# Performance work log

Measured on AMD Instinct MI355X. Metric: run time of the kernel, lower is better.

## Reference

```python
import jax, jax.numpy as jnp
import numpy as np

B, S, D, H, DH = 2, 2048, 1024, 16, 64
EPS = 1e-6


def setup_inputs() -> dict:
    key = jax.random.key(0)
    k0, k1, k2 = jax.random.split(key, 3)
    x = jax.random.normal(k0, (B, S, D), dtype=jnp.float32)
    mask = jnp.ones((B, S), dtype=bool)
    # NeoX-style rotary angles: half-dim inverse freqs, duplicated to rot_dim=DH
    inv_freq = 1.0 / (10000.0 ** (jnp.arange(0, DH, 2, dtype=jnp.float32) / DH))  # [DH/2]
    ang = jnp.arange(S, dtype=jnp.float32)[:, None] * inv_freq[None, :]            # [S, DH/2]
    freqs = jnp.concatenate([ang, ang], axis=-1)                                    # [S, DH]
    W_qkv = jax.random.normal(k1, (3 * D, D), dtype=jnp.float32) * (D ** -0.5)
    W_out = jax.random.normal(k2, (D, D), dtype=jnp.float32) * (D ** -0.5)
    q_gamma = jnp.ones((DH,), jnp.float32)
    q_beta = jnp.zeros((DH,), jnp.float32)
    k_gamma = jnp.ones((DH,), jnp.float32)
    k_beta = jnp.zeros((DH,), jnp.float32)
    return {"x": x, "mask": mask, "freqs": freqs, "W_qkv": W_qkv, "W_out": W_out,
            "q_gamma": q_gamma, "q_beta": q_beta, "k_gamma": k_gamma, "k_beta": k_beta}


def _layernorm(t, g, b):
    mu = t.mean(-1, keepdims=True)
    var = t.var(-1, keepdims=True)
    return (t - mu) * jax.lax.rsqrt(var + EPS) * g + b


def _rotate_half(t):
    t1, t2 = jnp.split(t, 2, axis=-1)
    return jnp.concatenate([-t2, t1], axis=-1)


def reference(x, mask, freqs, W_qkv, W_out, q_gamma, q_beta, k_gamma, k_beta):
    b, s, d = x.shape
    # fused QKV projection + split into heads: b n (h d) -> b h n d
    qkv = x @ W_qkv.T                                   # [b, s, 3d]
    q, k, v = jnp.split(qkv, 3, axis=-1)
    to_heads = lambda t: t.reshape(b, s, H, DH).transpose(0, 2, 1, 3)
    q, k, v = to_heads(q), to_heads(k), to_heads(v)      # [b, h, s, dh]
    # qk layernorm
    q = _layernorm(q, q_gamma, q_beta)
    k = _layernorm(k, k_gamma, k_beta)
    # rotary embedding (fp32 path in the original; inputs already fp32)
    cos = jnp.cos(freqs)[None, None]                      # [1, 1, s, dh]
    sin = jnp.sin(freqs)[None, None]
    q = q * cos + _rotate_half(q) * sin
    k = k * cos + _rotate_half(k) * sin
    # mask construction: key padding mask 'b j -> b 1 1 j' combined with causal
    key_mask = mask[:, None, None, :]                     # [b, 1, 1, s]
    causal = jnp.tril(jnp.ones((s, s), dtype=bool))       # [s, s]
    comb = key_mask & causal[None, None]                  # [b, 1, s, s]
    row_masked = ~comb.any(axis=-1)                       # [b, 1, s]
    comb = comb.at[..., 0].set(comb[..., 0] | row_masked)
    # SDPA
    scale = DH ** -0.5
    scores = jnp.einsum('bhid,bhjd->bhij', q, k) * scale  # [b, h, s, s]
    scores = jnp.where(comb, scores, jnp.finfo(scores.dtype).min)
    attn = jax.nn.softmax(scores, axis=-1)
    out = jnp.einsum('bhij,bhjd->bhid', attn, v)          # [b, h, s, dh]
    out = jnp.where(row_masked[..., None], 0.0, out)
    # merge heads + output projection
    out = out.transpose(0, 2, 1, 3).reshape(b, s, d)
    return out @ W_out.T
```

## Files before the change

### kernel.cpp

```cpp
#include <hip/hip_runtime.h>
#include <hip/hip_bf16.h>
#include <cstdint>

typedef unsigned short u16;
typedef __attribute__((ext_vector_type(8))) short s16x8;
typedef __attribute__((ext_vector_type(4))) float f32x4;
typedef __attribute__((ext_vector_type(16))) float f32x16;
typedef __attribute__((ext_vector_type(4))) unsigned int u32x4;
typedef __attribute__((ext_vector_type(2))) unsigned int u32x2;
typedef __attribute__((ext_vector_type(4))) u16 u16x4;

#define LOG2E 1.44269504088896340736f

__device__ __forceinline__ u16 f2b(float f) {
  union { float f; unsigned u; } v; v.f = f;
  unsigned r = v.u + 0x7FFF + ((v.u >> 16) & 1);
  return (u16)(r >> 16);
}

__device__ __forceinline__ float b2f(u16 u) {
  union { unsigned u; float f; } v; v.u = ((unsigned)u) << 16;
  return v.f;
}

__device__ __forceinline__ void gload_lds16(const u16* g, u16* l) {
  __builtin_amdgcn_global_load_lds((const __attribute__((address_space(1))) void*)g,
                                   (__attribute__((address_space(3))) void*)l, 16, 0, 0);
}

__global__ void cvt_bf16(const float* __restrict__ in, u16* __restrict__ out, int n) {
  int i = blockIdx.x * blockDim.x + threadIdx.x;
  if (i < n) out[i] = f2b(in[i]);
}

__global__ void trig_tab(const float* __restrict__ f, float* __restrict__ c,
                         float* __restrict__ s, int n) {
  int i = blockIdx.x * blockDim.x + threadIdx.x;
  if (i < n) { c[i] = cosf(f[i]); s[i] = sinf(f[i]); }
}

__global__ __launch_bounds__(256) void gemm_bt(const u16* __restrict__ A, const u16* __restrict__ B,
                                               float* __restrict__ C, int M, int N, int K) {
  __shared__ u16 sA[128 * 64];
  __shared__ u16 sB[128 * 64];
  const int nbn = N >> 7;
  int bx = blockIdx.x % nbn, by = blockIdx.x / nbn;
  int tid = threadIdx.x, w = tid >> 6, lane = tid & 63;
  int wr = (w >> 1) * 64, wc = (w & 1) * 64;
  int lr = lane >> 3, lc = lane & 7;
  f32x4 acc[4][4] = {};
  size_t arow = (size_t)(by * 128) * K;
  size_t brow = (size_t)(bx * 128) * K;
  for (int k0 = 0; k0 < K; k0 += 64) {
    __syncthreads();
    for (int c = 0; c < 4; ++c) {
      int r = w * 32 + c * 8;
      gload_lds16(A + arow + (size_t)(r + lr) * K + k0 + lc * 8, &sA[r * 64]);
      gload_lds16(B + brow + (size_t)(r + lr) * K + k0 + lc * 8, &sB[r * 64]);
    }
    __syncthreads();
    for (int kk = 0; kk < 64; kk += 32) {
      s16x8 af[4], bf[4];
      int ro = lane & 15, ko = kk + (lane >> 4) * 8;
      for (int m = 0; m < 4; ++m) af[m] = *(const s16x8*)&sA[(wr + m * 16 + ro) * 64 + ko];
      for (int n = 0; n < 4; ++n) bf[n] = *(const s16x8*)&sB[(wc + n * 16 + ro) * 64 + ko];
      for (int m = 0; m < 4; ++m)
        for (int n = 0; n < 4; ++n)
          acc[m][n] = __builtin_amdgcn_mfma_f32_16x16x32_bf16(af[m], bf[n], acc[m][n], 0, 0, 0);
    }
  }
  int ro = lane & 15, rg = lane >> 4;
  for (int m = 0; m < 4; ++m)
    for (int n = 0; n < 4; ++n) {
      int row = by * 128 + wr + m * 16 + rg * 4;
      int col = bx * 128 + wc + n * 16 + ro;
      float* cp = C + (size_t)row * N + col;
      for (int r = 0; r < 4; ++r) cp[(size_t)r * N] = acc[m][n][r];
    }
}

__global__ __launch_bounds__(256) void ln_rope(const float* __restrict__ qkv,
    const float* __restrict__ cosT, const float* __restrict__ sinT,
    const float* __restrict__ qg, const float* __restrict__ qb,
    const float* __restrict__ kg, const float* __restrict__ kb,
    u16* __restrict__ qo, u16* __restrict__ ko, u16* __restrict__ vo) {
  int gw = (blockIdx.x * 256 + threadIdx.x) >> 6;
  int lane = threadIdx.x & 63;
  int h = gw & 15, bs = gw >> 4;
  int s = bs & 2047, b = bs >> 11;
  const float* row = qkv + (size_t)bs * 3072;
  float qv = row[h * 64 + lane];
  float kv = row[1024 + h * 64 + lane];
  float vv = row[2048 + h * 64 + lane];

  float s1q = qv, s2q = qv * qv, s1k = kv, s2k = kv * kv;
  for (int off = 1; off < 64; off <<= 1) {
    s1q += __shfl_xor(s1q, off, 64); s2q += __shfl_xor(s2q, off, 64);
    s1k += __shfl_xor(s1k, off, 64); s2k += __shfl_xor(s2k, off, 64);
  }
  float muq = s1q * (1.f / 64.f), varq = s2q * (1.f / 64.f) - muq * muq;
  float muk = s1k * (1.f / 64.f), vark = s2k * (1.f / 64.f) - muk * muk;
  float qn = (qv - muq) * rsqrtf(varq + 1e-6f) * qg[lane] + qb[lane];
  float kn = (kv - muk) * rsqrtf(vark + 1e-6f) * kg[lane] + kb[lane];

  float cs = cosT[s * 64 + lane], sn = sinT[s * 64 + lane];
  float qh = __shfl_xor(qn, 32, 64); qh = (lane < 32) ? -qh : qh;
  float kh = __shfl_xor(kn, 32, 64); kh = (lane < 32) ? -kh : kh;
  float qr = (qn * cs + qh * sn) * 0.125f;
  float kr = kn * cs + kh * sn;

  size_t oidx = ((size_t)((b * 16 + h) * 2048 + s)) * 64 + lane;
  qo[oidx] = f2b(qr); ko[oidx] = f2b(kr); vo[oidx] = f2b(vv);
}

__global__ __launch_bounds__(256) void transpose_v(const u16* __restrict__ vi, u16* __restrict__ vt) {
  __shared__ __align__(16) u16 tile[64][72];
  int bh = blockIdx.x >> 5, st = blockIdx.x & 31;
  int t = threadIdx.x;
  const u16* src = vi + ((size_t)bh * 2048 + st * 64) * 64;
  int r = t & 63, c = (t >> 6) * 16;
  *(s16x8*)&tile[r][c]     = *(const s16x8*)(src + r * 64 + c);
  *(s16x8*)&tile[r][c + 8] = *(const s16x8*)(src + r * 64 + c + 8);
  __syncthreads();
  int dh = t & 63, so = (t >> 6) * 16;
  alignas(16) u16 buf[16];
  #pragma unroll
  for (int j = 0; j < 16; ++j) buf[j] = tile[so + j][dh];
  u16* dst = vt + ((size_t)bh * 64 + dh) * 2048 + st * 64 + so;
  *(s16x8*)dst       = *(const s16x8*)&buf[0];
  *(s16x8*)(dst + 8) = *(const s16x8*)&buf[8];
}

__global__ __launch_bounds__(256) void attn_fwd6(const u16* __restrict__ qp, const u16* __restrict__ kp,
                                                 const u16* __restrict__ vtp, u16* __restrict__ op) {
  __shared__ u16 sO[8][64][32];
  __shared__ float sM[8][32], sL[8][32];
  int bid = blockIdx.x;
  int xcd = bid & 7, j = bid >> 3;
  int bh = 4 * xcd + (j >> 5), pr = j & 31;
  int tid = threadIdx.x, w = tid >> 6, l = tid & 63;
  int ql = l & 31, h5 = l >> 5;
  const int A = pr, Bs = 63 - pr;
  int b = bh >> 4, h = bh & 15;
  const u16* qptr = qp + (size_t)bh * 2048 * 64;
  const u16* kptr = kp + (size_t)bh * 2048 * 64;
  const u16* vptr = vtp + (size_t)bh * 64 * 2048;

  s16x8 qfA[4], qfB[4];
  {
    const u16* qrA = qptr + (size_t)(A * 32 + ql) * 64 + h5 * 8;
    const u16* qrB = qptr + (size_t)(Bs * 32 + ql) * 64 + h5 * 8;
    #pragma unroll
    for (int t = 0; t < 4; ++t) { qfA[t] = *(const s16x8*)(qrA + 16 * t);
                                  qfB[t] = *(const s16x8*)(qrB + 16 * t); }
  }
  f32x16 oA0 = {}, oA1 = {}, oB0 = {}, oB1 = {};
  float mA = -INFINITY, lA = 0.f, mB = -INFINITY, lB = 0.f;

  auto tile = [&](const s16x8* qf, float& m, float& lsum, f32x16& o0, f32x16& o1,
                  s16x8 k0, s16x8 k1, s16x8 k2, s16x8 k3,
                  s16x8 v00, s16x8 v01, s16x8 v10, s16x8 v11, int kt, int strip) {
    f32x16 sc = {};
    sc = __builtin_amdgcn_mfma_f32_32x32x16_bf16(k0, qf[0], sc, 0, 0, 0);
    sc = __builtin_amdgcn_mfma_f32_32x32x16_bf16(k1, qf[1], sc, 0, 0, 0);
    sc = __builtin_amdgcn_mfma_f32_32x32x16_bf16(k2, qf[2], sc, 0, 0, 0);
    sc = __builtin_amdgcn_mfma_f32_32x32x16_bf16(k3, qf[3], sc, 0, 0, 0);

    if (kt == strip) {
      #pragma unroll
      for (int r = 0; r < 16; ++r) {
        int kloc = (r & 3) + 8 * (r >> 2) + 4 * h5;
        sc[r] = (kloc > ql) ? -INFINITY : sc[r];
      }
    }
    float t8[8], t4[4];
    #pragma unroll
    for (int i = 0; i < 8; ++i) t8[i] = fmaxf(sc[2 * i], sc[2 * i + 1]);
    #pragma unroll
    for (int i = 0; i < 4; ++i) t4[i] = fmaxf(t8[2 * i], t8[2 * i + 1]);
    float mx = fmaxf(fmaxf(t4[0], t4[1]), fmaxf(t4[2], t4[3]));
    mx = fmaxf(mx, __shfl_xor(mx, 32, 64));

    if (__any(mx > m)) {
      float mn = fmaxf(m, mx);
      float alpha = __builtin_amdgcn_exp2f((m - mn) * LOG2E);
      #pragma unroll
      for (int r = 0; r < 16; ++r) { o0[r] *= alpha; o1[r] *= alpha; }
      lsum *= alpha;
      m = mn;
    }
    float rs = 0.f;
    #pragma unroll
    for (int r = 0; r < 16; ++r) {
      float p = __builtin_amdgcn_exp2f((sc[r] - m) * LOG2E);
      sc[r] = p; rs += p;
    }
    rs += __shfl_xor(rs, 32, 64);
    lsum += rs;

    unsigned wd[8];
    #pragma unroll
    for (int i = 0; i < 8; ++i)
      asm("v_cvt_pk_bf16_f32 %0, %1, %2" : "=v"(wd[i]) : "v"(sc[2 * i]), "v"(sc[2 * i + 1]));
    u32x2 r02 = __builtin_amdgcn_permlane32_swap(wd[0], wd[2], false, false);
    u32x2 r13 = __builtin_amdgcn_permlane32_swap(wd[1], wd[3], false, false);
    u32x2 r46 = __builtin_amdgcn_permlane32_swap(wd[4], wd[6], false, false);
    u32x2 r57 = __builtin_amdgcn_permlane32_swap(wd[5], wd[7], false, false);
    u32x4 t0v = {r02[0], r13[0], r02[1], r13[1]};
    u32x4 t1v = {r46[0], r57[0], r46[1], r57[1]};
    s16x8 pa0 = __builtin_bit_cast(s16x8, t0v);
    s16x8 pa1 = __builtin_bit_cast(s16x8, t1v);

    o0 = __builtin_amdgcn_mfma_f32_32x32x16_bf16(v00, pa0, o0, 0, 0, 0);
    o0 = __builtin_amdgcn_mfma_f32_32x32x16_bf16(v01, pa1, o0, 0, 0, 0);
    o1 = __builtin_amdgcn_mfma_f32_32x32x16_bf16(v10, pa0, o1, 0, 0, 0);
    o1 = __builtin_amdgcn_mfma_f32_32x32x16_bf16(v11, pa1, o1, 0, 0, 0);
  };

  for (int kt = w; kt <= Bs; kt += 4) {
    const u16* kr = kptr + (size_t)(kt * 32 + ql) * 64 + h5 * 8;
    s16x8 k0 = *(const s16x8*)(kr);
    s16x8 k1 = *(const s16x8*)(kr + 16);
    s16x8 k2 = *(const s16x8*)(kr + 32);
    s16x8 k3 = *(const s16x8*)(kr + 48);
    const u16* vr = vptr + (size_t)ql * 2048 + kt * 32 + h5 * 8;
    s16x8 v00 = *(const s16x8*)(vr);
    s16x8 v01 = *(const s16x8*)(vr + 16);
    s16x8 v10 = *(const s16x8*)(vr + 32 * 2048);
    s16x8 v11 = *(const s16x8*)(vr + 32 * 2048 + 16);

    tile(qfB, mB, lB, oB0, oB1, k0, k1, k2, k3, v00, v01, v10, v11, kt, Bs);
    if (kt <= A)
      tile(qfA, mA, lA, oA0, oA1, k0, k1, k2, k3, v00, v01, v10, v11, kt, A);
  }

  if (h5 == 0) {
    sM[w * 2 + 0][ql] = mA; sL[w * 2 + 0][ql] = lA;
    sM[w * 2 + 1][ql] = mB; sL[w * 2 + 1][ql] = lB;
  }
  #pragma unroll
  for (int r = 0; r < 16; ++r) {
    int dh = (r & 3) + 8 * (r >> 2) + 4 * h5;
    sO[w * 2 + 0][dh][ql]      = f2b(oA0[r]);
    sO[w * 2 + 0][dh + 32][ql] = f2b(oA1[r]);
    sO[w * 2 + 1][dh][ql]      = f2b(oB0[r]);
    sO[w * 2 + 1][dh + 32][ql] = f2b(oB1[r]);
  }
  __syncthreads();

  {
    int q = tid & 31, dg = tid >> 5;
    #pragma unroll
    for (int s = 0; s < 2; ++s) {
      float m0 = sM[0 * 2 + s][q], m1 = sM[1 * 2 + s][q];
      float m2 = sM[2 * 2 + s][q], m3 = sM[3 * 2 + s][q];
      float mg = fmaxf(fmaxf(m0, m1), fmaxf(m2, m3));
      float e0 = __builtin_amdgcn_exp2f((m0 - mg) * LOG2E);
      float e1 = __builtin_amdgcn_exp2f((m1 - mg) * LOG2E);
      float e2 = __builtin_amdgcn_exp2f((m2 - mg) * LOG2E);
      float e3 = __builtin_amdgcn_exp2f((m3 - mg) * LOG2E);
      float lg = e0 * sL[0 * 2 + s][q] + e1 * sL[1 * 2 + s][q]
               + e2 * sL[2 * 2 + s][q] + e3 * sL[3 * 2 + s][q];
      float inv = 1.f / lg;
      alignas(16) u16 ob[8];
      #pragma unroll
      for (int jj = 0; jj < 8; ++jj) {
        int dh = dg * 8 + jj;
        float acc = e0 * b2f(sO[0 * 2 + s][dh][q]) + e1 * b2f(sO[1 * 2 + s][dh][q])
                  + e2 * b2f(sO[2 * 2 + s][dh][q]) + e3 * b2f(sO[3 * 2 + s][dh][q]);
        ob[jj] = f2b(acc * inv);
      }
      int q0s = (s ? Bs : A) * 32;
      u16* dst = op + ((size_t)(b * 2048 + q0s + q)) * 1024 + h * 64 + dg * 8;
      *(u16x4*)dst       = *(const u16x4*)&ob[0];
      *(u16x4*)(dst + 4) = *(const u16x4*)&ob[4];
    }
  }
}

extern "C" void kernel_launch(void* const* d_in, const int* in_sizes, int n_in,
                              void* d_out, int out_size, void* d_ws, size_t ws_size,
                              hipStream_t stream) {
  const float* x     = (const float*)d_in[0];
  const float* freqs = (const float*)d_in[2];
  const float* Wqkv  = (const float*)d_in[3];
  const float* Wout  = (const float*)d_in[4];
  const float* qg    = (const float*)d_in[5];
  const float* qb    = (const float*)d_in[6];
  const float* kg    = (const float*)d_in[7];
  const float* kb    = (const float*)d_in[8];
  float* out = (float*)d_out;

  u16* xb    = (u16*)d_ws;
  u16* wqkvb = xb + 4194304;
  u16* woutb = wqkvb + 3145728;
  float* cosT = (float*)(woutb + 1048576);
  float* sinT = cosT + 131072;
  float* qkv  = sinT + 131072;
  u16* qo = (u16*)(qkv + 12582912);
  u16* ko = qo + 4194304;
  u16* vo = ko + 4194304;
  u16* ao = vo + 4194304;
  u16* vt = (u16*)qkv;

  cvt_bf16<<<(4194304 + 255) / 256, 256, 0, stream>>>(x, xb, 4194304);
  cvt_bf16<<<(3145728 + 255) / 256, 256, 0, stream>>>(Wqkv, wqkvb, 3145728);
  cvt_bf16<<<(1048576 + 255) / 256, 256, 0, stream>>>(Wout, woutb, 1048576);
  trig_tab<<<(131072 + 255) / 256, 256, 0, stream>>>(freqs, cosT, sinT, 131072);

  gemm_bt<<<(4096 / 128) * (3072 / 128), 256, 0, stream>>>(xb, wqkvb, qkv, 4096, 3072, 1024);
  ln_rope<<<65536 / 4, 256, 0, stream>>>(qkv, cosT, sinT, qg, qb, kg, kb, qo, ko, vo);
  transpose_v<<<32 * 32, 256, 0, stream>>>(vo, vt);
  attn_fwd6<<<1024, 256, 0, stream>>>(qo, ko, vt, ao);
  gemm_bt<<<(4096 / 128) * (1024 / 128), 256, 0, stream>>>(ao, woutb, out, 4096, 1024, 1024);
}
```

Baseline: 261.6 us.

## Fuse QK layernorm and rotary into QKV GEMM epilogue; pair key tiles in attention

```diff
diff --git a/kernel.cpp b/kernel.cpp
--- a/kernel.cpp
+++ b/kernel.cpp
@@ -33,10 +33,9 @@
   if (i < n) out[i] = f2b(in[i]);
 }
 
-__global__ void trig_tab(const float* __restrict__ f, float* __restrict__ c,
-                         float* __restrict__ s, int n) {
+__global__ void trig2_tab(const float* __restrict__ f, float2* __restrict__ t, int n) {
   int i = blockIdx.x * blockDim.x + threadIdx.x;
-  if (i < n) { c[i] = cosf(f[i]); s[i] = sinf(f[i]); }
+  if (i < n) { t[i] = make_float2(cosf(f[i]), sinf(f[i])); }
 }
 
 __global__ __launch_bounds__(256) void gemm_bt(const u16* __restrict__ A, const u16* __restrict__ B,
@@ -79,38 +78,91 @@
     }
 }
 
-__global__ __launch_bounds__(256) void ln_rope(const float* __restrict__ qkv,
-    const float* __restrict__ cosT, const float* __restrict__ sinT,
+__global__ __launch_bounds__(256) void gemm_qkv_lnrope(
+    const u16* __restrict__ A, const u16* __restrict__ B, const float2* __restrict__ trig,
     const float* __restrict__ qg, const float* __restrict__ qb,
     const float* __restrict__ kg, const float* __restrict__ kb,
     u16* __restrict__ qo, u16* __restrict__ ko, u16* __restrict__ vo) {
-  int gw = (blockIdx.x * 256 + threadIdx.x) >> 6;
-  int lane = threadIdx.x & 63;
-  int h = gw & 15, bs = gw >> 4;
-  int s = bs & 2047, b = bs >> 11;
-  const float* row = qkv + (size_t)bs * 3072;
-  float qv = row[h * 64 + lane];
-  float kv = row[1024 + h * 64 + lane];
-  float vv = row[2048 + h * 64 + lane];
-
-  float s1q = qv, s2q = qv * qv, s1k = kv, s2k = kv * kv;
-  for (int off = 1; off < 64; off <<= 1) {
-    s1q += __shfl_xor(s1q, off, 64); s2q += __shfl_xor(s2q, off, 64);
-    s1k += __shfl_xor(s1k, off, 64); s2k += __shfl_xor(s2k, off, 64);
-  }
-  float muq = s1q * (1.f / 64.f), varq = s2q * (1.f / 64.f) - muq * muq;
-  float muk = s1k * (1.f / 64.f), vark = s2k * (1.f / 64.f) - muk * muk;
-  float qn = (qv - muq) * rsqrtf(varq + 1e-6f) * qg[lane] + qb[lane];
-  float kn = (kv - muk) * rsqrtf(vark + 1e-6f) * kg[lane] + kb[lane];
-
-  float cs = cosT[s * 64 + lane], sn = sinT[s * 64 + lane];
-  float qh = __shfl_xor(qn, 32, 64); qh = (lane < 32) ? -qh : qh;
-  float kh = __shfl_xor(kn, 32, 64); kh = (lane < 32) ? -kh : kh;
-  float qr = (qn * cs + qh * sn) * 0.125f;
-  float kr = kn * cs + kh * sn;
-
-  size_t oidx = ((size_t)((b * 16 + h) * 2048 + s)) * 64 + lane;
-  qo[oidx] = f2b(qr); ko[oidx] = f2b(kr); vo[oidx] = f2b(vv);
+  const int K = 1024;
+  __shared__ u16 sA[128 * 64];
+  __shared__ u16 sB[128 * 64];
+  int bx = blockIdx.x % 24, by = blockIdx.x / 24;
+  int tid = threadIdx.x, w = tid >> 6, lane = tid & 63;
+  int wr = (w >> 1) * 64, wc = (w & 1) * 64;
+  int lr = lane >> 3, lc = lane & 7;
+  f32x4 acc[4][4] = {};
+  size_t arow = (size_t)(by * 128) * K;
+  size_t brow = (size_t)(bx * 128) * K;
+  for (int k0 = 0; k0 < K; k0 += 64) {
+    __syncthreads();
+    for (int c = 0; c < 4; ++c) {
+      int r = w * 32 + c * 8;
+      gload_lds16(A + arow + (size_t)(r + lr) * K + k0 + lc * 8, &sA[r * 64]);
+      gload_lds16(B + brow + (size_t)(r + lr) * K + k0 + lc * 8, &sB[r * 64]);
+    }
+    __syncthreads();
+    for (int kk = 0; kk < 64; kk += 32) {
+      s16x8 af[4], bf[4];
+      int ro = lane & 15, ko = kk + (lane >> 4) * 8;
+      for (int m = 0; m < 4; ++m) af[m] = *(const s16x8*)&sA[(wr + m * 16 + ro) * 64 + ko];
+      for (int n = 0; n < 4; ++n) bf[n] = *(const s16x8*)&sB[(wc + n * 16 + ro) * 64 + ko];
+      for (int m = 0; m < 4; ++m)
+        for (int n = 0; n < 4; ++n)
+          acc[m][n] = __builtin_amdgcn_mfma_f32_16x16x32_bf16(af[m], bf[n], acc[m][n], 0, 0, 0);
+    }
+  }
+  int ro = lane & 15, rg = lane >> 4;
+  int gc0 = bx * 128 + wc;
+  int sec = gc0 >> 10;
+  int h = (gc0 & 1023) >> 6;
+  if (sec == 2) {
+    #pragma unroll
+    for (int m = 0; m < 4; ++m)
+      #pragma unroll
+      for (int r = 0; r < 4; ++r) {
+        int row = by * 128 + wr + m * 16 + rg * 4 + r;
+        int s = row & 2047, bb = row >> 11;
+        u16* dst = vo + ((size_t)((bb * 16 + h) * 2048 + s)) * 64;
+        #pragma unroll
+        for (int n = 0; n < 4; ++n) dst[n * 16 + ro] = f2b(acc[m][n][r]);
+      }
+  } else {
+    const float* gmm = sec ? kg : qg;
+    const float* bet = sec ? kb : qb;
+    float gv[4], bv[4];
+    #pragma unroll
+    for (int n = 0; n < 4; ++n) { gv[n] = gmm[n * 16 + ro]; bv[n] = bet[n * 16 + ro]; }
+    float qscale = sec == 0 ? 0.125f : 1.0f;
+    u16* base = sec == 0 ? qo : ko;
+    #pragma unroll
+    for (int m = 0; m < 4; ++m)
+      #pragma unroll
+      for (int r = 0; r < 4; ++r) {
+        float v0 = acc[m][0][r], v1 = acc[m][1][r], v2 = acc[m][2][r], v3 = acc[m][3][r];
+        float s1 = v0 + v1 + v2 + v3;
+        float s2 = v0 * v0 + v1 * v1 + v2 * v2 + v3 * v3;
+        #pragma unroll
+        for (int off = 1; off < 16; off <<= 1) {
+          s1 += __shfl_xor(s1, off, 64);
+          s2 += __shfl_xor(s2, off, 64);
+        }
+        float mu = s1 * (1.f / 64.f), var = s2 * (1.f / 64.f) - mu * mu;
+        float rr = rsqrtf(var + 1e-6f);
+        float nrm[4];
+        #pragma unroll
+        for (int n = 0; n < 4; ++n) nrm[n] = (acc[m][n][r] - mu) * rr * gv[n] + bv[n];
+        int row = by * 128 + wr + m * 16 + rg * 4 + r;
+        int s = row & 2047, bb = row >> 11;
+        const float2* tr = trig + (size_t)s * 64;
+        u16* dst = base + ((size_t)((bb * 16 + h) * 2048 + s)) * 64;
+        #pragma unroll
+        for (int n = 0; n < 4; ++n) {
+          float2 cs = tr[n * 16 + ro];
+          float rot = (n < 2) ? -nrm[n + 2] : nrm[n - 2];
+          dst[n * 16 + ro] = f2b((nrm[n] * cs.x + rot * cs.y) * qscale);
+        }
+      }
+  }
 }
 
 __global__ __launch_bounds__(256) void transpose_v(const u16* __restrict__ vi, u16* __restrict__ vt) {
@@ -131,7 +183,7 @@
   *(s16x8*)(dst + 8) = *(const s16x8*)&buf[8];
 }
 
-__global__ __launch_bounds__(256) void attn_fwd6(const u16* __restrict__ qp, const u16* __restrict__ kp,
+__global__ __launch_bounds__(256) void attn_fwd7(const u16* __restrict__ qp, const u16* __restrict__ kp,
                                                  const u16* __restrict__ vtp, u16* __restrict__ op) {
   __shared__ u16 sO[8][64][32];
   __shared__ float sM[8][32], sL[8][32];
@@ -157,47 +209,28 @@
   f32x16 oA0 = {}, oA1 = {}, oB0 = {}, oB1 = {};
   float mA = -INFINITY, lA = 0.f, mB = -INFINITY, lB = 0.f;
 
-  auto tile = [&](const s16x8* qf, float& m, float& lsum, f32x16& o0, f32x16& o1,
-                  s16x8 k0, s16x8 k1, s16x8 k2, s16x8 k3,
-                  s16x8 v00, s16x8 v01, s16x8 v10, s16x8 v11, int kt, int strip) {
-    f32x16 sc = {};
-    sc = __builtin_amdgcn_mfma_f32_32x32x16_bf16(k0, qf[0], sc, 0, 0, 0);
-    sc = __builtin_amdgcn_mfma_f32_32x32x16_bf16(k1, qf[1], sc, 0, 0, 0);
-    sc = __builtin_amdgcn_mfma_f32_32x32x16_bf16(k2, qf[2], sc, 0, 0, 0);
-    sc = __builtin_amdgcn_mfma_f32_32x32x16_bf16(k3, qf[3], sc, 0, 0, 0);
-
-    if (kt == strip) {
-      #pragma unroll
-      for (int r = 0; r < 16; ++r) {
-        int kloc = (r & 3) + 8 * (r >> 2) + 4 * h5;
-        sc[r] = (kloc > ql) ? -INFINITY : sc[r];
-      }
-    }
+  auto qk = [&](const s16x8* qf, const s16x8* kf) {
+    f32x16 s = {};
+    #pragma unroll
+    for (int t = 0; t < 4; ++t) s = __builtin_amdgcn_mfma_f32_32x32x16_bf16(kf[t], qf[t], s, 0, 0, 0);
+    return s;
+  };
+  auto maskd = [&](f32x16& sc) {
+    #pragma unroll
+    for (int r = 0; r < 16; ++r) {
+      int kloc = (r & 3) + 8 * (r >> 2) + 4 * h5;
+      sc[r] = (kloc > ql) ? -INFINITY : sc[r];
+    }
+  };
+  auto vmax = [&](const f32x16& sc) {
     float t8[8], t4[4];
     #pragma unroll
     for (int i = 0; i < 8; ++i) t8[i] = fmaxf(sc[2 * i], sc[2 * i + 1]);
     #pragma unroll
     for (int i = 0; i < 4; ++i) t4[i] = fmaxf(t8[2 * i], t8[2 * i + 1]);
-    float mx = fmaxf(fmaxf(t4[0], t4[1]), fmaxf(t4[2], t4[3]));
-    mx = fmaxf(mx, __shfl_xor(mx, 32, 64));
-
-    if (__any(mx > m)) {
-      float mn = fmaxf(m, mx);
-      float alpha = __builtin_amdgcn_exp2f((m - mn) * LOG2E);
-      #pragma unroll
-      for (int r = 0; r < 16; ++r) { o0[r] *= alpha; o1[r] *= alpha; }
-      lsum *= alpha;
-      m = mn;
-    }
-    float rs = 0.f;
-    #pragma unroll
-    for (int r = 0; r < 16; ++r) {
-      float p = __builtin_amdgcn_exp2f((sc[r] - m) * LOG2E);
-      sc[r] = p; rs += p;
-    }
-    rs += __shfl_xor(rs, 32, 64);
-    lsum += rs;
-
+    return fmaxf(fmaxf(t4[0], t4[1]), fmaxf(t4[2], t4[3]));
+  };
+  auto pconv = [&](const f32x16& sc, s16x8& pa0, s16x8& pa1) {
     unsigned wd[8];
     #pragma unroll
     for (int i = 0; i < 8; ++i)
@@ -208,31 +241,101 @@
     u32x2 r57 = __builtin_amdgcn_permlane32_swap(wd[5], wd[7], false, false);
     u32x4 t0v = {r02[0], r13[0], r02[1], r13[1]};
     u32x4 t1v = {r46[0], r57[0], r46[1], r57[1]};
-    s16x8 pa0 = __builtin_bit_cast(s16x8, t0v);
-    s16x8 pa1 = __builtin_bit_cast(s16x8, t1v);
-
-    o0 = __builtin_amdgcn_mfma_f32_32x32x16_bf16(v00, pa0, o0, 0, 0, 0);
-    o0 = __builtin_amdgcn_mfma_f32_32x32x16_bf16(v01, pa1, o0, 0, 0, 0);
-    o1 = __builtin_amdgcn_mfma_f32_32x32x16_bf16(v10, pa0, o1, 0, 0, 0);
-    o1 = __builtin_amdgcn_mfma_f32_32x32x16_bf16(v11, pa1, o1, 0, 0, 0);
-  };
-
-  for (int kt = w; kt <= Bs; kt += 4) {
+    pa0 = __builtin_bit_cast(s16x8, t0v);
+    pa1 = __builtin_bit_cast(s16x8, t1v);
+  };
+  auto soft = [&](float& m, float& lsum, f32x16& o0, f32x16& o1,
+                  f32x16& sx, f32x16& sy, bool has_y,
+                  const s16x8* vx, const s16x8* vy) {
+    float mx = vmax(sx);
+    if (has_y) mx = fmaxf(mx, vmax(sy));
+    mx = fmaxf(mx, __shfl_xor(mx, 32, 64));
+    if (__any(mx > m)) {
+      float mn = fmaxf(m, mx);
+      float al = __builtin_amdgcn_exp2f((m - mn) * LOG2E);
+      #pragma unroll
+      for (int r = 0; r < 16; ++r) { o0[r] *= al; o1[r] *= al; }
+      lsum *= al;
+      m = mn;
+    }
+    float rs = 0.f;
+    #pragma unroll
+    for (int r = 0; r < 16; ++r) {
+      float p = __builtin_amdgcn_exp2f((sx[r] - m) * LOG2E);
+      sx[r] = p; rs += p;
+    }
+    if (has_y)
+      #pragma unroll
+      for (int r = 0; r < 16; ++r) {
+        float p = __builtin_amdgcn_exp2f((sy[r] - m) * LOG2E);
+        sy[r] = p; rs += p;
+      }
+    lsum += rs;
+    s16x8 pa0, pa1;
+    pconv(sx, pa0, pa1);
+    o0 = __builtin_amdgcn_mfma_f32_32x32x16_bf16(vx[0], pa0, o0, 0, 0, 0);
+    o0 = __builtin_amdgcn_mfma_f32_32x32x16_bf16(vx[1], pa1, o0, 0, 0, 0);
+    o1 = __builtin_amdgcn_mfma_f32_32x32x16_bf16(vx[2], pa0, o1, 0, 0, 0);
+    o1 = __builtin_amdgcn_mfma_f32_32x32x16_bf16(vx[3], pa1, o1, 0, 0, 0);
+    if (has_y) {
+      s16x8 pb0, pb1;
+      pconv(sy, pb0, pb1);
+      o0 = __builtin_amdgcn_mfma_f32_32x32x16_bf16(vy[0], pb0, o0, 0, 0, 0);
+      o0 = __builtin_amdgcn_mfma_f32_32x32x16_bf16(vy[1], pb1, o0, 0, 0, 0);
+      o1 = __builtin_amdgcn_mfma_f32_32x32x16_bf16(vy[2], pb0, o1, 0, 0, 0);
+      o1 = __builtin_amdgcn_mfma_f32_32x32x16_bf16(vy[3], pb1, o1, 0, 0, 0);
+    }
+  };
+  auto ldk = [&](s16x8* kf, int kt) {
     const u16* kr = kptr + (size_t)(kt * 32 + ql) * 64 + h5 * 8;
-    s16x8 k0 = *(const s16x8*)(kr);
-    s16x8 k1 = *(const s16x8*)(kr + 16);
-    s16x8 k2 = *(const s16x8*)(kr + 32);
-    s16x8 k3 = *(const s16x8*)(kr + 48);
+    #pragma unroll
+    for (int t = 0; t < 4; ++t) kf[t] = *(const s16x8*)(kr + 16 * t);
+  };
+  auto ldv = [&](s16x8* vf, int kt) {
     const u16* vr = vptr + (size_t)ql * 2048 + kt * 32 + h5 * 8;
-    s16x8 v00 = *(const s16x8*)(vr);
-    s16x8 v01 = *(const s16x8*)(vr + 16);
-    s16x8 v10 = *(const s16x8*)(vr + 32 * 2048);
-    s16x8 v11 = *(const s16x8*)(vr + 32 * 2048 + 16);
-
-    tile(qfB, mB, lB, oB0, oB1, k0, k1, k2, k3, v00, v01, v10, v11, kt, Bs);
-    if (kt <= A)
-      tile(qfA, mA, lA, oA0, oA1, k0, k1, k2, k3, v00, v01, v10, v11, kt, A);
-  }
+    vf[0] = *(const s16x8*)(vr);
+    vf[1] = *(const s16x8*)(vr + 16);
+    vf[2] = *(const s16x8*)(vr + 32 * 2048);
+    vf[3] = *(const s16x8*)(vr + 32 * 2048 + 16);
+  };
+
+  int kt = w;
+  while (kt + 4 <= Bs) {
+    s16x8 kx[4], ky[4], vx[4], vy[4];
+    ldk(kx, kt); ldk(ky, kt + 4);
+    ldv(vx, kt); ldv(vy, kt + 4);
+    {
+      f32x16 sx = qk(qfB, kx), sy = qk(qfB, ky);
+      if (kt + 4 == Bs) maskd(sy);
+      soft(mB, lB, oB0, oB1, sx, sy, true, vx, vy);
+    }
+    if (kt <= A) {
+      f32x16 sx = qk(qfA, kx);
+      if (kt + 4 <= A) {
+        f32x16 sy = qk(qfA, ky);
+        if (kt + 4 == A) maskd(sy);
+        soft(mA, lA, oA0, oA1, sx, sy, true, vx, vy);
+      } else {
+        if (kt == A) maskd(sx);
+        soft(mA, lA, oA0, oA1, sx, sx, false, vx, vx);
+      }
+    }
+    kt += 8;
+  }
+  if (kt <= Bs) {
+    s16x8 kx[4], vx[4];
+    ldk(kx, kt); ldv(vx, kt);
+    f32x16 sx = qk(qfB, kx);
+    if (kt == Bs) maskd(sx);
+    soft(mB, lB, oB0, oB1, sx, sx, false, vx, vx);
+    if (kt <= A) {
+      f32x16 sa = qk(qfA, kx);
+      if (kt == A) maskd(sa);
+      soft(mA, lA, oA0, oA1, sa, sa, false, vx, vx);
+    }
+  }
+  lA += __shfl_xor(lA, 32, 64);
+  lB += __shfl_xor(lB, 32, 64);
 
   if (h5 == 0) {
     sM[w * 2 + 0][ql] = mA; sL[w * 2 + 0][ql] = lA;
@@ -294,23 +397,20 @@
   u16* xb    = (u16*)d_ws;
   u16* wqkvb = xb + 4194304;
   u16* woutb = wqkvb + 3145728;
-  float* cosT = (float*)(woutb + 1048576);
-  float* sinT = cosT + 131072;
-  float* qkv  = sinT + 131072;
-  u16* qo = (u16*)(qkv + 12582912);
+  float2* trig2 = (float2*)(woutb + 1048576);
+  u16* qo = (u16*)(trig2 + 131072);
   u16* ko = qo + 4194304;
   u16* vo = ko + 4194304;
   u16* ao = vo + 4194304;
-  u16* vt = (u16*)qkv;
+  u16* vt = ao + 4194304;
 
   cvt_bf16<<<(4194304 + 255) / 256, 256, 0, stream>>>(x, xb, 4194304);
   cvt_bf16<<<(3145728 + 255) / 256, 256, 0, stream>>>(Wqkv, wqkvb, 3145728);
   cvt_bf16<<<(1048576 + 255) / 256, 256, 0, stream>>>(Wout, woutb, 1048576);
-  trig_tab<<<(131072 + 255) / 256, 256, 0, stream>>>(freqs, cosT, sinT, 131072);
-
-  gemm_bt<<<(4096 / 128) * (3072 / 128), 256, 0, stream>>>(xb, wqkvb, qkv, 4096, 3072, 1024);
-  ln_rope<<<65536 / 4, 256, 0, stream>>>(qkv, cosT, sinT, qg, qb, kg, kb, qo, ko, vo);
+  trig2_tab<<<(131072 + 255) / 256, 256, 0, stream>>>(freqs, trig2, 131072);
+
+  gemm_qkv_lnrope<<<24 * 32, 256, 0, stream>>>(xb, wqkvb, trig2, qg, qb, kg, kb, qo, ko, vo);
   transpose_v<<<32 * 32, 256, 0, stream>>>(vo, vt);
-  attn_fwd6<<<1024, 256, 0, stream>>>(qo, ko, vt, ao);
+  attn_fwd7<<<1024, 256, 0, stream>>>(qo, ko, vt, ao);
   gemm_bt<<<(4096 / 128) * (1024 / 128), 256, 0, stream>>>(ao, woutb, out, 4096, 1024, 1024);
 }
```

New measurement: 253.1 us. 3.2% less time.
